# Kernel tuning notes

Hardware: AMD Instinct MI355X
Metric: run time of the kernel (lower is better)

Reference implementation:

```python
import jax, jax.numpy as jnp
import numpy as np

B, C, H, W = 8, 1, 384, 384
P, D, NH, L, E, HF = 16, 768, 12, 12, 4, 3072
Hp, Wp = H // P, W // P
N = Hp * Wp            # 576 tokens
DH = D // NH           # 64 per head
EPS = 1e-5


def setup_inputs() -> dict:
    key = jax.random.key(0)
    ks = jax.random.split(key, 10)
    g = lambda k, shp: (0.02 * jax.random.normal(k, shp, dtype=jnp.float32))
    return {
        "x": jax.random.normal(ks[0], (B, C, H, W), dtype=jnp.float32),
        "patch_w": g(ks[1], (D, C * P * P)),        # Conv2d(k=16,s=16) == unfold+matmul
        "patch_b": jnp.zeros((D,), jnp.float32),
        "pos_embed": g(ks[2], (1, N, D)),
        "ln1_g": jnp.ones((L, D), jnp.float32),
        "ln1_b": jnp.zeros((L, D), jnp.float32),
        "qkv_w": g(ks[3], (L, 3 * D, D)),           # torch MHA in_proj_weight
        "qkv_b": jnp.zeros((L, 3 * D), jnp.float32),
        "out_w": g(ks[4], (L, D, D)),
        "out_b": jnp.zeros((L, D), jnp.float32),
        "ln2_g": jnp.ones((L, D), jnp.float32),
        "ln2_b": jnp.zeros((L, D), jnp.float32),
        "gate_w": g(ks[5], (L, E, D)),
        "gate_b": jnp.zeros((L, E), jnp.float32),
        "w1": g(ks[6], (L, E, HF, D)),
        "b1": jnp.zeros((L, E, HF), jnp.float32),
        "w2": g(ks[7], (L, E, D, HF)),
        "b2": jnp.zeros((L, E, D), jnp.float32),
    }


def _ln(x, g, b):
    m = jnp.mean(x, -1, keepdims=True)
    v = jnp.var(x, -1, keepdims=True)
    return (x - m) * jax.lax.rsqrt(v + EPS) * g + b


def _layer(t, prm):
    (l1g, l1b, qw, qb, ow, ob, l2g, l2b, gw, gb, W1, B1, W2, B2) = prm
    # --- MHA (pre-LN, residual) ---
    h = _ln(t, l1g, l1b)
    qkv = h @ qw.T + qb                                   # [B,N,3D]
    q, k, v = jnp.split(qkv, 3, axis=-1)
    q = q.reshape(B, N, NH, DH).transpose(0, 2, 1, 3)     # [B,NH,N,DH]
    k = k.reshape(B, N, NH, DH).transpose(0, 2, 1, 3)
    v = v.reshape(B, N, NH, DH).transpose(0, 2, 1, 3)
    att = jax.nn.softmax(jnp.einsum('bhnd,bhmd->bhnm', q, k) / jnp.sqrt(jnp.float32(DH)), axis=-1)
    a = jnp.einsum('bhnm,bhmd->bhnd', att, v).transpose(0, 2, 1, 3).reshape(B, N, D)
    t = t + a @ ow.T + ob
    # --- MoE FFN, top_k=1: raw gate logits used as combine weights ---
    h2 = _ln(t, l2g, l2b)
    scores = h2 @ gw.T + gb                               # [B,N,E]
    idx = jnp.argmax(scores, axis=-1)                     # [B,N] chosen expert
    wgt = jnp.max(scores, axis=-1)                        # [B,N] raw logit weight
    hid = jax.nn.gelu(jnp.einsum('bnd,ehd->benh', h2, W1) + B1[None, :, None, :], approximate=False)
    y = jnp.einsum('benh,edh->bend', hid, W2) + B2[None, :, None, :]   # [B,E,N,D]
    sel = jax.nn.one_hot(idx, E, dtype=t.dtype) * wgt[..., None]       # [B,N,E]
    t = t + jnp.einsum('bend,bne->bnd', y, sel)
    return t, None


def reference(x, patch_w, patch_b, pos_embed, ln1_g, ln1_b, qkv_w, qkv_b,
              out_w, out_b, ln2_g, ln2_b, gate_w, gate_b, w1, b1, w2, b2):
    # patch embed: Conv2d(kernel=stride=P) == non-overlapping unfold + matmul
    patches = x.reshape(B, C, Hp, P, Wp, P).transpose(0, 2, 4, 1, 3, 5).reshape(B, N, C * P * P)
    tok = patches @ patch_w.T + patch_b + pos_embed
    layer = jax.checkpoint(_layer)
    tok, _ = jax.lax.scan(layer, tok,
                          (ln1_g, ln1_b, qkv_w, qkv_b, out_w, out_b,
                           ln2_g, ln2_b, gate_w, gate_b, w1, b1, w2, b2))
    # rearrange 'b (h w) c -> b c h w'
    return tok.reshape(B, Hp, Wp, D).transpose(0, 3, 1, 2)
```

## Files before the change

kernel.cpp:

```cpp
#include <hip/hip_runtime.h>
#include <cmath>

#define TOK 4608
#define DMODEL 768

typedef __attribute__((ext_vector_type(8))) _Float16 f16x8;
typedef __attribute__((ext_vector_type(4))) float f32x4;

__device__ __forceinline__ float gelu_exact(float x) {
    return 0.5f * x * (1.0f + erff(x * 0.70710678118654752440f));
}

__device__ __forceinline__ void cvt2(float x, unsigned short& h, unsigned short& m)
{
    _Float16 hf = (_Float16)x;
    float r = (x - (float)hf) * 2048.0f;
    _Float16 mf = (_Float16)r;
    h = __builtin_bit_cast(unsigned short, hf);
    m = __builtin_bit_cast(unsigned short, mf);
}

__device__ __forceinline__ void cvt2_pack8(const float4 a, const float4 b,
                                           uint4& H, uint4& M)
{
    unsigned short h[8], m[8];
    cvt2(a.x, h[0], m[0]); cvt2(a.y, h[1], m[1]);
    cvt2(a.z, h[2], m[2]); cvt2(a.w, h[3], m[3]);
    cvt2(b.x, h[4], m[4]); cvt2(b.y, h[5], m[5]);
    cvt2(b.z, h[6], m[6]); cvt2(b.w, h[7], m[7]);
    H = (uint4){ (unsigned)h[0] | ((unsigned)h[1] << 16), (unsigned)h[2] | ((unsigned)h[3] << 16),
                 (unsigned)h[4] | ((unsigned)h[5] << 16), (unsigned)h[6] | ((unsigned)h[7] << 16) };
    M = (uint4){ (unsigned)m[0] | ((unsigned)m[1] << 16), (unsigned)m[2] | ((unsigned)m[3] << 16),
                 (unsigned)m[4] | ((unsigned)m[5] << 16), (unsigned)m[6] | ((unsigned)m[7] << 16) };
}

__global__ __launch_bounds__(256)
void im2col_kernel(const float* __restrict__ x, float* __restrict__ patches)
{
    int idx = blockIdx.x*256 + threadIdx.x;
    int k = idx & 255, tokid = idx >> 8;
    int b = tokid / 576, n = tokid % 576;
    int hp = n / 24, wp = n % 24;
    patches[idx] = x[(size_t)b*147456 + (size_t)(hp*16 + (k >> 4))*384 + wp*16 + (k & 15)];
}

__global__ __launch_bounds__(256)
void ln_kernel(const float* __restrict__ in, float* __restrict__ out,
               const float* __restrict__ g, const float* __restrict__ bta)
{
    int tokid = blockIdx.x;
    const float* xr = in + (size_t)tokid*768;
    int t = threadIdx.x;
    float v0 = xr[t], v1 = xr[t+256], v2 = xr[t+512];
    float s = v0+v1+v2, q = v0*v0+v1*v1+v2*v2;
    for (int off = 32; off > 0; off >>= 1) {
        s += __shfl_down(s, off);
        q += __shfl_down(q, off);
    }
    __shared__ float ss[4], sq[4];
    int wv = t >> 6, ln = t & 63;
    if (ln == 0) { ss[wv] = s; sq[wv] = q; }
    __syncthreads();
    float ts = ss[0]+ss[1]+ss[2]+ss[3];
    float tq = sq[0]+sq[1]+sq[2]+sq[3];
    float mean = ts * (1.f/768.f);
    float var  = tq * (1.f/768.f) - mean*mean;
    float inv  = rsqrtf(var + 1e-5f);
    float* orow = out + (size_t)tokid*768;
    orow[t]     = (v0-mean)*inv*g[t]     + bta[t];
    orow[t+256] = (v1-mean)*inv*g[t+256] + bta[t+256];
    orow[t+512] = (v2-mean)*inv*g[t+512] + bta[t+512];
}

__global__ __launch_bounds__(256)
void ln2_gate_kernel(const float* __restrict__ in, float* __restrict__ out,
                     const float* __restrict__ g, const float* __restrict__ bta,
                     const float* __restrict__ gw, const float* __restrict__ gb,
                     float* __restrict__ wgt, int* __restrict__ lists,
                     int* __restrict__ counts)
{
    int tokid = blockIdx.x;
    const float* xr = in + (size_t)tokid*768;
    int t = threadIdx.x;
    float v0 = xr[t], v1 = xr[t+256], v2 = xr[t+512];
    float s = v0+v1+v2, q = v0*v0+v1*v1+v2*v2;
    for (int off = 32; off > 0; off >>= 1) {
        s += __shfl_down(s, off);
        q += __shfl_down(q, off);
    }
    __shared__ float ss[4], sq[4];
    __shared__ float red[4][4];
    int wv = t >> 6, ln = t & 63;
    if (ln == 0) { ss[wv] = s; sq[wv] = q; }
    __syncthreads();
    float ts = ss[0]+ss[1]+ss[2]+ss[3];
    float tq = sq[0]+sq[1]+sq[2]+sq[3];
    float mean = ts * (1.f/768.f);
    float var  = tq * (1.f/768.f) - mean*mean;
    float inv  = rsqrtf(var + 1e-5f);
    float y0 = (v0-mean)*inv*g[t]     + bta[t];
    float y1 = (v1-mean)*inv*g[t+256] + bta[t+256];
    float y2 = (v2-mean)*inv*g[t+512] + bta[t+512];
    float* orow = out + (size_t)tokid*768;
    orow[t] = y0; orow[t+256] = y1; orow[t+512] = y2;

    float p0, p1, p2, p3;
    p0 = fmaf(y0, gw[t], 0.f);        p0 = fmaf(y1, gw[t+256], p0);        p0 = fmaf(y2, gw[t+512], p0);
    p1 = fmaf(y0, gw[768+t], 0.f);    p1 = fmaf(y1, gw[768+t+256], p1);    p1 = fmaf(y2, gw[768+t+512], p1);
    p2 = fmaf(y0, gw[1536+t], 0.f);   p2 = fmaf(y1, gw[1536+t+256], p2);   p2 = fmaf(y2, gw[1536+t+512], p2);
    p3 = fmaf(y0, gw[2304+t], 0.f);   p3 = fmaf(y1, gw[2304+t+256], p3);   p3 = fmaf(y2, gw[2304+t+512], p3);
    for (int off = 32; off > 0; off >>= 1) {
        p0 += __shfl_down(p0, off);
        p1 += __shfl_down(p1, off);
        p2 += __shfl_down(p2, off);
        p3 += __shfl_down(p3, off);
    }
    if (ln == 0) { red[wv][0]=p0; red[wv][1]=p1; red[wv][2]=p2; red[wv][3]=p3; }
    __syncthreads();
    if (t == 0) {
        float sc[4];
        #pragma unroll
        for (int e = 0; e < 4; ++e)
            sc[e] = red[0][e]+red[1][e]+red[2][e]+red[3][e] + gb[e];
        int best = 0; float bv = sc[0];
        #pragma unroll
        for (int e = 1; e < 4; ++e) if (sc[e] > bv) { bv = sc[e]; best = e; }
        wgt[tokid] = bv;
        int pos = atomicAdd(&counts[best], 1);
        lists[best*TOK + pos] = tokid;
    }
}

template<bool SWZ>
__global__ __launch_bounds__(256, 2)
void gemm_big(const float* __restrict__ A, const float* __restrict__ Bw,
              const float* __restrict__ bias, float* __restrict__ C,
              int M, int Nout, int K, int ldA, int ldC, int mode,
              const int* __restrict__ lists, const int* __restrict__ counts,
              const float* __restrict__ wgt)
{
    int Meff = M;
    const int* gather = nullptr;
    if (counts) {
        int e = blockIdx.z;
        Meff   = counts[e];
        gather = lists + e * TOK;
        Bw    += (size_t)e * Nout * K;
        bias  += (size_t)e * Nout;
    }
    int m0, n0;
    if constexpr (SWZ) {
        int gx  = gridDim.x;
        int nwg = gx * gridDim.y;
        int bid = blockIdx.y * gx + blockIdx.x;
        bid = (bid & 7) * (nwg >> 3) + (bid >> 3);
        m0 = (bid / gx) << 7; n0 = (bid % gx) << 7;
    } else {
        m0 = blockIdx.y << 7; n0 = blockIdx.x << 7;
    }
    if (m0 >= Meff) return;

    __shared__ unsigned short Ah[128][40];
    __shared__ unsigned short Am[128][40];
    __shared__ unsigned short Bh[128][40];
    __shared__ unsigned short Bm[128][40];

    int t = threadIdx.x;
    int srow = t >> 1;
    int koff = (t & 1) << 4;

    int ar = m0 + srow;
    long agrow = -1;
    if (ar < Meff) agrow = gather ? gather[ar] : ar;
    const float* Asrc = (agrow >= 0) ? (A + (size_t)agrow*ldA + koff) : nullptr;
    const float* Bsrc = Bw + (size_t)(n0 + srow)*K + koff;

    int lane = t & 63;
    int wv   = t >> 6;
    int wm   = (wv >> 1) << 6;
    int wn   = (wv & 1) << 6;
    int r16  = lane & 15;
    int g    = lane >> 4;

    f32x4 acc1[4][4], acc2[4][4];
    #pragma unroll
    for (int i = 0; i < 4; ++i)
        #pragma unroll
        for (int j = 0; j < 4; ++j) {
            acc1[i][j] = (f32x4){0.f, 0.f, 0.f, 0.f};
            acc2[i][j] = (f32x4){0.f, 0.f, 0.f, 0.f};
        }

    float4 ra[4], rb[4];
    ra[0] = ra[1] = ra[2] = ra[3] = make_float4(0.f, 0.f, 0.f, 0.f);

    auto load_tile = [&](int k0) {
        if (Asrc) {
            ra[0] = *(const float4*)(Asrc + k0);
            ra[1] = *(const float4*)(Asrc + k0 + 4);
            ra[2] = *(const float4*)(Asrc + k0 + 8);
            ra[3] = *(const float4*)(Asrc + k0 + 12);
        }
        rb[0] = *(const float4*)(Bsrc + k0);
        rb[1] = *(const float4*)(Bsrc + k0 + 4);
        rb[2] = *(const float4*)(Bsrc + k0 + 8);
        rb[3] = *(const float4*)(Bsrc + k0 + 12);
    };

    load_tile(0);

    for (int k0 = 0; k0 < K; k0 += 32) {
        __syncthreads();
        {
            uint4 H, M_;
            cvt2_pack8(ra[0], ra[1], H, M_);
            *(uint4*)&Ah[srow][koff]   = H;
            *(uint4*)&Am[srow][koff]   = M_;
            cvt2_pack8(ra[2], ra[3], H, M_);
            *(uint4*)&Ah[srow][koff+8] = H;
            *(uint4*)&Am[srow][koff+8] = M_;
            cvt2_pack8(rb[0], rb[1], H, M_);
            *(uint4*)&Bh[srow][koff]   = H;
            *(uint4*)&Bm[srow][koff]   = M_;
            cvt2_pack8(rb[2], rb[3], H, M_);
            *(uint4*)&Bh[srow][koff+8] = H;
            *(uint4*)&Bm[srow][koff+8] = M_;
        }
        __syncthreads();
        if (k0 + 32 < K) load_tile(k0 + 32);

        f16x8 fah[4], fam[4];
        #pragma unroll
        for (int i = 0; i < 4; ++i) {
            int ml = wm + i*16 + r16;
            fah[i] = *(const f16x8*)&Ah[ml][g*8];
            fam[i] = *(const f16x8*)&Am[ml][g*8];
        }
        #pragma unroll
        for (int j = 0; j < 4; ++j) {
            int nl = wn + j*16 + r16;
            f16x8 fbh = *(const f16x8*)&Bh[nl][g*8];
            f16x8 fbm = *(const f16x8*)&Bm[nl][g*8];
            #pragma unroll
            for (int i = 0; i < 4; ++i) {
                acc1[i][j] = __builtin_amdgcn_mfma_f32_16x16x32_f16(fah[i], fbh, acc1[i][j], 0, 0, 0);
                acc2[i][j] = __builtin_amdgcn_mfma_f32_16x16x32_f16(fah[i], fbm, acc2[i][j], 0, 0, 0);
                acc2[i][j] = __builtin_amdgcn_mfma_f32_16x16x32_f16(fam[i], fbh, acc2[i][j], 0, 0, 0);
            }
        }
    }

    const float MS = 1.0f / 2048.0f;
    float biasv[4];
    #pragma unroll
    for (int j = 0; j < 4; ++j) biasv[j] = bias[n0 + wn + j*16 + r16];

    #pragma unroll
    for (int i = 0; i < 4; ++i) {
        int mb = m0 + wm + i*16 + (g << 2);
        #pragma unroll
        for (int r = 0; r < 4; ++r) {
            int m = mb + r;
            if (m >= Meff) continue;
            int row = gather ? gather[m] : m;
            size_t rowoff = (size_t)row*ldC + n0 + wn + r16;
            float w = (mode == 3) ? wgt[row] : 0.f;
            #pragma unroll
            for (int j = 0; j < 4; ++j) {
                float val = acc1[i][j][r] + acc2[i][j][r] * MS + biasv[j];
                size_t off = rowoff + j*16;
                if      (mode == 0) C[off] = val;
                else if (mode == 1) C[off] += val;
                else if (mode == 2) C[off] = gelu_exact(val);
                else if (mode == 3) C[off] += w * val;
                else C[off] = val + wgt[(size_t)(row % 576)*768 + n0 + wn + j*16 + r16];
            }
        }
    }
}

template<bool SWZ>
__global__ __launch_bounds__(256, 2)
void gemm_small(const float* __restrict__ A, const float* __restrict__ Bw,
                const float* __restrict__ bias, float* __restrict__ C,
                int M, int Nout, int K, int ldA, int ldC, int mode,
                const int* __restrict__ lists, const int* __restrict__ counts,
                const float* __restrict__ wgt)
{
    int Meff = M;
    const int* gather = nullptr;
    if (counts) {
        int e = blockIdx.z;
        Meff   = counts[e];
        gather = lists + e * TOK;
        Bw    += (size_t)e * Nout * K;
        bias  += (size_t)e * Nout;
    }
    int m0, n0;
    if constexpr (SWZ) {
        int gx  = gridDim.x;
        int nwg = gx * gridDim.y;
        int bid = blockIdx.y * gx + blockIdx.x;
        bid = (bid & 7) * (nwg >> 3) + (bid >> 3);
        m0 = (bid / gx) << 6; n0 = (bid % gx) << 6;
    } else {
        m0 = blockIdx.y << 6; n0 = blockIdx.x << 6;
    }
    if (m0 >= Meff) return;

    __shared__ unsigned short Ah[64][72];
    __shared__ unsigned short Am[64][72];
    __shared__ unsigned short Bh[64][72];
    __shared__ unsigned short Bm[64][72];

    int t = threadIdx.x;
    int srow  = t >> 1;
    int khalf = (t & 1) << 5;
    bool isA = srow < 64;
    int row  = isA ? srow : (srow - 64);

    const float* src = nullptr;
    if (isA) {
        int ar = m0 + row;
        if (ar < Meff) {
            long agrow = gather ? gather[ar] : ar;
            src = A + (size_t)agrow*ldA + khalf;
        }
    } else {
        src = Bw + (size_t)(n0 + row)*K + khalf;
    }

    int lane = t & 63;
    int wv   = t >> 6;
    int wm   = (wv >> 1) << 5;
    int wn   = (wv & 1) << 5;
    int r16  = lane & 15;
    int g    = lane >> 4;

    f32x4 acc1[2][2], acc2[2][2];
    #pragma unroll
    for (int i = 0; i < 2; ++i)
        #pragma unroll
        for (int j = 0; j < 2; ++j) {
            acc1[i][j] = (f32x4){0.f, 0.f, 0.f, 0.f};
            acc2[i][j] = (f32x4){0.f, 0.f, 0.f, 0.f};
        }

    float4 rr[8];
    #pragma unroll
    for (int i = 0; i < 8; ++i) rr[i] = make_float4(0.f, 0.f, 0.f, 0.f);

    auto load_tile = [&](int k0) {
        if (src) {
            #pragma unroll
            for (int i = 0; i < 8; ++i) rr[i] = *(const float4*)(src + k0 + 4*i);
        }
    };

    load_tile(0);

    for (int k0 = 0; k0 < K; k0 += 64) {
        __syncthreads();
        {
            unsigned short (*Xh)[72] = isA ? Ah : Bh;
            unsigned short (*Xm)[72] = isA ? Am : Bm;
            #pragma unroll
            for (int i = 0; i < 8; i += 2) {
                uint4 H, M_;
                cvt2_pack8(rr[i], rr[i+1], H, M_);
                *(uint4*)&Xh[row][khalf + 4*i] = H;
                *(uint4*)&Xm[row][khalf + 4*i] = M_;
            }
        }
        __syncthreads();
        if (k0 + 64 < K) load_tile(k0 + 64);

        #pragma unroll
        for (int ks = 0; ks < 2; ++ks) {
            f16x8 fah[2], fam[2];
            #pragma unroll
            for (int i = 0; i < 2; ++i) {
                int ml = wm + i*16 + r16;
                fah[i] = *(const f16x8*)&Ah[ml][ks*32 + g*8];
                fam[i] = *(const f16x8*)&Am[ml][ks*32 + g*8];
            }
            #pragma unroll
            for (int j = 0; j < 2; ++j) {
                int nl = wn + j*16 + r16;
                f16x8 fbh = *(const f16x8*)&Bh[nl][ks*32 + g*8];
                f16x8 fbm = *(const f16x8*)&Bm[nl][ks*32 + g*8];
                #pragma unroll
                for (int i = 0; i < 2; ++i) {
                    acc1[i][j] = __builtin_amdgcn_mfma_f32_16x16x32_f16(fah[i], fbh, acc1[i][j], 0, 0, 0);
                    acc2[i][j] = __builtin_amdgcn_mfma_f32_16x16x32_f16(fah[i], fbm, acc2[i][j], 0, 0, 0);
                    acc2[i][j] = __builtin_amdgcn_mfma_f32_16x16x32_f16(fam[i], fbh, acc2[i][j], 0, 0, 0);
                }
            }
        }
    }

    const float MS = 1.0f / 2048.0f;
    float biasv[2];
    #pragma unroll
    for (int j = 0; j < 2; ++j) biasv[j] = bias[n0 + wn + j*16 + r16];

    #pragma unroll
    for (int i = 0; i < 2; ++i) {
        int mb = m0 + wm + i*16 + (g << 2);
        #pragma unroll
        for (int r = 0; r < 4; ++r) {
            int m = mb + r;
            if (m >= Meff) continue;
            int rowc = gather ? gather[m] : m;
            size_t rowoff = (size_t)rowc*ldC + n0 + wn + r16;
            float w = (mode == 3) ? wgt[rowc] : 0.f;
            #pragma unroll
            for (int j = 0; j < 2; ++j) {
                float val = acc1[i][j][r] + acc2[i][j][r] * MS + biasv[j];
                size_t off = rowoff + j*16;
                if      (mode == 0) C[off] = val;
                else if (mode == 1) C[off] += val;
                else if (mode == 2) C[off] = gelu_exact(val);
                else if (mode == 3) C[off] += w * val;
                else C[off] = val + wgt[(size_t)(rowc % 576)*768 + n0 + wn + j*16 + r16];
            }
        }
    }
}

__global__ __launch_bounds__(256)
void attn_kernel(const float* __restrict__ qkv, float* __restrict__ attn)
{
    int q0 = blockIdx.x << 6;
    int h  = blockIdx.y;
    int b  = blockIdx.z;
    const float* base = qkv + (size_t)b * 576 * 2304;
    int qoff = h << 6, koff = 768 + (h << 6), voff = 1536 + (h << 6);

    __shared__ unsigned short Qh[64][72], Qm[64][72];
    __shared__ unsigned short Kh[64][72], Km[64][72];
    __shared__ unsigned short Vth[64][72], Vtm[64][72];
    __shared__ unsigned short Ph[64][72], Pm[64][72];

    int t    = threadIdx.x;
    int lane = t & 63;
    int wq   = t >> 6;
    int l15  = lane & 15;
    int g    = lane >> 4;

    int srow = t >> 2;
    int sq   = t & 3;

    {
        const float* src = &base[(size_t)(q0 + srow)*2304 + qoff + (sq << 4)];
        #pragma unroll
        for (int k = 0; k < 16; k += 4) {
            float4 v = *(const float4*)(src + k);
            ushort4 hh, mm;
            cvt2(v.x, hh.x, mm.x); cvt2(v.y, hh.y, mm.y);
            cvt2(v.z, hh.z, mm.z); cvt2(v.w, hh.w, mm.w);
            *(ushort4*)&Qh[srow][(sq << 4) + k] = hh;
            *(ushort4*)&Qm[srow][(sq << 4) + k] = mm;
        }
    }
    __syncthreads();

    f16x8 fqh[2], fqm[2];
    #pragma unroll
    for (int ks = 0; ks < 2; ++ks) {
        fqh[ks] = *(const f16x8*)&Qh[wq*16 + l15][ks*32 + g*8];
        fqm[ks] = *(const f16x8*)&Qm[wq*16 + l15][ks*32 + g*8];
    }

    float4 rk[4], rv[4];
    {
        const float* ks_ = &base[(size_t)srow*2304 + koff + (sq << 4)];
        const float* vs_ = &base[(size_t)srow*2304 + voff + (sq << 2)];
        #pragma unroll
        for (int k = 0; k < 4; ++k) rk[k] = *(const float4*)(ks_ + 4*k);
        #pragma unroll
        for (int k = 0; k < 4; ++k) rv[k] = *(const float4*)(vs_ + 16*k);
    }

    f32x4 o1[4], o2[4];
    #pragma unroll
    for (int df = 0; df < 4; ++df) {
        o1[df] = (f32x4){0.f,0.f,0.f,0.f};
        o2[df] = (f32x4){0.f,0.f,0.f,0.f};
    }
    float m_[4] = {-3.4e38f,-3.4e38f,-3.4e38f,-3.4e38f};
    float l_[4] = {0.f,0.f,0.f,0.f};
    const float MS = 1.0f / 2048.0f;

    for (int j0 = 0; j0 < 576; j0 += 64) {
        __syncthreads();
        #pragma unroll
        for (int k = 0; k < 4; ++k) {
            ushort4 hh, mm;
            cvt2(rk[k].x, hh.x, mm.x); cvt2(rk[k].y, hh.y, mm.y);
            cvt2(rk[k].z, hh.z, mm.z); cvt2(rk[k].w, hh.w, mm.w);
            *(ushort4*)&Kh[srow][(sq << 4) + 4*k] = hh;
            *(ushort4*)&Km[srow][(sq << 4) + 4*k] = mm;
        }
        #pragma unroll
        for (int k = 0; k < 4; ++k) {
            ushort4 hh, mm;
            cvt2(rv[k].x, hh.x, mm.x); cvt2(rv[k].y, hh.y, mm.y);
            cvt2(rv[k].z, hh.z, mm.z); cvt2(rv[k].w, hh.w, mm.w);
            int dbase = (sq << 2) + (k << 4);
            Vth[dbase+0][srow] = hh.x; Vtm[dbase+0][srow] = mm.x;
            Vth[dbase+1][srow] = hh.y; Vtm[dbase+1][srow] = mm.y;
            Vth[dbase+2][srow] = hh.z; Vtm[dbase+2][srow] = mm.z;
            Vth[dbase+3][srow] = hh.w; Vtm[dbase+3][srow] = mm.w;
        }
        __syncthreads();
        int jn = j0 + 64;
        if (jn < 576) {
            const float* ks_ = &base[(size_t)(jn + srow)*2304 + koff + (sq << 4)];
            const float* vs_ = &base[(size_t)(jn + srow)*2304 + voff + (sq << 2)];
            #pragma unroll
            for (int k = 0; k < 4; ++k) rk[k] = *(const float4*)(ks_ + 4*k);
            #pragma unroll
            for (int k = 0; k < 4; ++k) rv[k] = *(const float4*)(vs_ + 16*k);
        }

        f32x4 s1[4], s2[4];
        #pragma unroll
        for (int jf = 0; jf < 4; ++jf) {
            s1[jf] = (f32x4){0.f,0.f,0.f,0.f};
            s2[jf] = (f32x4){0.f,0.f,0.f,0.f};
        }
        #pragma unroll
        for (int jf = 0; jf < 4; ++jf) {
            #pragma unroll
            for (int ks = 0; ks < 2; ++ks) {
                f16x8 fkh = *(const f16x8*)&Kh[jf*16 + l15][ks*32 + g*8];
                f16x8 fkm = *(const f16x8*)&Km[jf*16 + l15][ks*32 + g*8];
                s1[jf] = __builtin_amdgcn_mfma_f32_16x16x32_f16(fqh[ks], fkh, s1[jf], 0, 0, 0);
                s2[jf] = __builtin_amdgcn_mfma_f32_16x16x32_f16(fqh[ks], fkm, s2[jf], 0, 0, 0);
                s2[jf] = __builtin_amdgcn_mfma_f32_16x16x32_f16(fqm[ks], fkh, s2[jf], 0, 0, 0);
            }
        }
        float p[4][4];
        #pragma unroll
        for (int jf = 0; jf < 4; ++jf)
            #pragma unroll
            for (int r = 0; r < 4; ++r)
                p[jf][r] = (s1[jf][r] + s2[jf][r]*MS) * 0.125f;

        #pragma unroll
        for (int r = 0; r < 4; ++r) {
            float tm = fmaxf(fmaxf(p[0][r], p[1][r]), fmaxf(p[2][r], p[3][r]));
            #pragma unroll
            for (int off = 8; off > 0; off >>= 1) tm = fmaxf(tm, __shfl_xor(tm, off, 16));
            float mn = fmaxf(m_[r], tm);
            float f  = expf(m_[r] - mn);
            m_[r] = mn;
            l_[r] *= f;
            #pragma unroll
            for (int df = 0; df < 4; ++df) { o1[df][r] *= f; o2[df][r] *= f; }
            float ps = 0.f;
            #pragma unroll
            for (int jf = 0; jf < 4; ++jf) {
                p[jf][r] = expf(p[jf][r] - mn);
                ps += p[jf][r];
            }
            #pragma unroll
            for (int off = 8; off > 0; off >>= 1) ps += __shfl_xor(ps, off, 16);
            l_[r] += ps;
        }
        #pragma unroll
        for (int jf = 0; jf < 4; ++jf)
            #pragma unroll
            for (int r = 0; r < 4; ++r) {
                unsigned short ph, pm;
                cvt2(p[jf][r], ph, pm);
                Ph[wq*16 + g*4 + r][jf*16 + l15] = ph;
                Pm[wq*16 + g*4 + r][jf*16 + l15] = pm;
            }

        #pragma unroll
        for (int ks = 0; ks < 2; ++ks) {
            f16x8 fph = *(const f16x8*)&Ph[wq*16 + l15][ks*32 + g*8];
            f16x8 fpm = *(const f16x8*)&Pm[wq*16 + l15][ks*32 + g*8];
            #pragma unroll
            for (int df = 0; df < 4; ++df) {
                f16x8 fvh = *(const f16x8*)&Vth[df*16 + l15][ks*32 + g*8];
                f16x8 fvm = *(const f16x8*)&Vtm[df*16 + l15][ks*32 + g*8];
                o1[df] = __builtin_amdgcn_mfma_f32_16x16x32_f16(fph, fvh, o1[df], 0, 0, 0);
                o2[df] = __builtin_amdgcn_mfma_f32_16x16x32_f16(fph, fvm, o2[df], 0, 0, 0);
                o2[df] = __builtin_amdgcn_mfma_f32_16x16x32_f16(fpm, fvh, o2[df], 0, 0, 0);
            }
        }
    }

    #pragma unroll
    for (int r = 0; r < 4; ++r) {
        float inv = 1.f / l_[r];
        size_t row = (size_t)(b*576 + q0 + wq*16 + g*4 + r)*768 + qoff + l15;
        #pragma unroll
        for (int df = 0; df < 4; ++df)
            attn[row + df*16] = (o1[df][r] + o2[df][r]*MS) * inv;
    }
}

__global__ void zero_counts48(int* counts) { if (threadIdx.x < 48) counts[threadIdx.x] = 0; }

__global__ __launch_bounds__(256)
void out_transpose(const float* __restrict__ tok, float* __restrict__ out)
{
    int idx = blockIdx.x*256 + threadIdx.x;
    int wp = idx % 24;
    int hp = (idx / 24) % 24;
    int d  = (idx / 576) % 768;
    int b  = idx / (576*768);
    out[idx] = tok[(size_t)(b*576 + hp*24 + wp)*768 + d];
}

extern "C" void kernel_launch(void* const* d_in, const int* in_sizes, int n_in,
                              void* d_out, int out_size, void* d_ws, size_t ws_size,
                              hipStream_t stream)
{
    const float* x       = (const float*)d_in[0];
    const float* patch_w = (const float*)d_in[1];
    const float* patch_b = (const float*)d_in[2];
    const float* pos     = (const float*)d_in[3];
    const float* ln1_g   = (const float*)d_in[4];
    const float* ln1_b   = (const float*)d_in[5];
    const float* qkv_w   = (const float*)d_in[6];
    const float* qkv_b   = (const float*)d_in[7];
    const float* out_w   = (const float*)d_in[8];
    const float* out_b   = (const float*)d_in[9];
    const float* ln2_g   = (const float*)d_in[10];
    const float* ln2_b   = (const float*)d_in[11];
    const float* gate_w  = (const float*)d_in[12];
    const float* gate_b  = (const float*)d_in[13];
    const float* w1      = (const float*)d_in[14];
    const float* b1      = (const float*)d_in[15];
    const float* w2      = (const float*)d_in[16];
    const float* b2      = (const float*)d_in[17];
    float* out = (float*)d_out;

    float* ws    = (float*)d_ws;
    float* tok   = ws;
    float* h     = ws + 3538944;
    float* scr   = ws + 7077888;
    float* qkv   = scr;
    float* attn  = scr + 10616832;
    float* hid   = scr;
    float* patches = scr;
    float* wgt   = ws + 21233664;
    int*   lists = (int*)(ws + 21238272);
    int*   counts= (int*)(ws + 21256704);

    zero_counts48<<<1, 64, 0, stream>>>(counts);

    im2col_kernel<<<4608, 256, 0, stream>>>(x, patches);
    gemm_small<true><<<dim3(12,72,1), 256, 0, stream>>>(patches, patch_w, patch_b, tok,
                                                        4608, 768, 256, 256, 768, 4,
                                                        nullptr, nullptr, pos);

    for (int l = 0; l < 12; ++l) {
        int* counts_l = counts + l*4;
        ln_kernel<<<4608, 256, 0, stream>>>(tok, h, ln1_g + l*768, ln1_b + l*768);
        gemm_big<true><<<dim3(18,36,1), 256, 0, stream>>>(h, qkv_w + (size_t)l*1769472,
                                                          qkv_b + l*2304, qkv,
                                                          4608, 2304, 768, 768, 2304, 0,
                                                          nullptr, nullptr, nullptr);
        attn_kernel<<<dim3(9,12,8), 256, 0, stream>>>(qkv, attn);
        gemm_small<true><<<dim3(12,72,1), 256, 0, stream>>>(attn, out_w + (size_t)l*589824,
                                                            out_b + l*768, tok,
                                                            4608, 768, 768, 768, 768, 1,
                                                            nullptr, nullptr, nullptr);
        ln2_gate_kernel<<<4608, 256, 0, stream>>>(tok, h, ln2_g + l*768, ln2_b + l*768,
                                                  gate_w + l*3072, gate_b + l*4,
                                                  wgt, lists, counts_l);
        gemm_big<false><<<dim3(24,36,4), 256, 0, stream>>>(h, w1 + (size_t)l*9437184,
                                                           b1 + (size_t)l*4*3072, hid,
                                                           4608, 3072, 768, 768, 3072, 2,
                                                           lists, counts_l, nullptr);
        gemm_small<false><<<dim3(12,72,4), 256, 0, stream>>>(hid, w2 + (size_t)l*9437184,
                                                             b2 + (size_t)l*4*768, tok,
                                                             4608, 768, 3072, 3072, 768, 3,
                                                             lists, counts_l, wgt);
    }
    out_transpose<<<13824, 256, 0, stream>>>(tok, out);
}
```

Measured before the change: 8.169 ms.

## Replace GEMM kernels with 256x128-tile 512-thread wide GEMM for all layer matmuls

Replaces the 128x128-tile, 256-thread GEMM with a 256x128-tile, 512-thread variant (8 waves) that reuses each B tile across twice as many rows. It is used for the QKV, out-projection and both MoE expert GEMMs, replacing gemm_small for the N=768 cases. The XCD swizzle is generalised to grids whose block count is not a multiple of 8. The intent is fewer B reloads and less per-block overhead, at the cost of more LDS per block, fewer blocks for the N=768 GEMMs, and more wasted rows on partially filled expert tiles.

```diff
diff --git a/kernel.cpp b/kernel.cpp
--- a/kernel.cpp
+++ b/kernel.cpp
@@ -132,12 +132,12 @@
 }
 
 template<bool SWZ>
-__global__ __launch_bounds__(256, 2)
-void gemm_big(const float* __restrict__ A, const float* __restrict__ Bw,
-              const float* __restrict__ bias, float* __restrict__ C,
-              int M, int Nout, int K, int ldA, int ldC, int mode,
-              const int* __restrict__ lists, const int* __restrict__ counts,
-              const float* __restrict__ wgt)
+__global__ __launch_bounds__(512, 2)
+void gemm_wide(const float* __restrict__ A, const float* __restrict__ Bw,
+               const float* __restrict__ bias, float* __restrict__ C,
+               int M, int Nout, int K, int ldA, int ldC, int mode,
+               const int* __restrict__ lists, const int* __restrict__ counts,
+               const float* __restrict__ wgt)
 {
     int Meff = M;
     const int* gather = nullptr;
@@ -148,32 +148,34 @@
         Bw    += (size_t)e * Nout * K;
         bias  += (size_t)e * Nout;
     }
-    int m0, n0;
+    int gx  = gridDim.x;
+    int bid = blockIdx.y * gx + blockIdx.x;
     if constexpr (SWZ) {
-        int gx  = gridDim.x;
         int nwg = gx * gridDim.y;
-        int bid = blockIdx.y * gx + blockIdx.x;
-        bid = (bid & 7) * (nwg >> 3) + (bid >> 3);
-        m0 = (bid / gx) << 7; n0 = (bid % gx) << 7;
-    } else {
-        m0 = blockIdx.y << 7; n0 = blockIdx.x << 7;
-    }
+        int qq = nwg >> 3, rr8 = nwg & 7;
+        int xcd = bid & 7, idx = bid >> 3;
+        bid = (xcd < rr8 ? xcd*(qq+1) : rr8*(qq+1) + (xcd-rr8)*qq) + idx;
+    }
+    int m0 = (bid / gx) << 8;
+    int n0 = (bid % gx) << 7;
     if (m0 >= Meff) return;
 
-    __shared__ unsigned short Ah[128][40];
-    __shared__ unsigned short Am[128][40];
+    __shared__ unsigned short Ah[256][40];
+    __shared__ unsigned short Am[256][40];
     __shared__ unsigned short Bh[128][40];
     __shared__ unsigned short Bm[128][40];
 
     int t = threadIdx.x;
-    int srow = t >> 1;
-    int koff = (t & 1) << 4;
+    int srow  = t >> 1;
+    int koff  = (t & 1) << 4;
+    int brow  = t >> 2;
+    int bkoff = (t & 3) << 3;
 
     int ar = m0 + srow;
     long agrow = -1;
     if (ar < Meff) agrow = gather ? gather[ar] : ar;
     const float* Asrc = (agrow >= 0) ? (A + (size_t)agrow*ldA + koff) : nullptr;
-    const float* Bsrc = Bw + (size_t)(n0 + srow)*K + koff;
+    const float* Bsrc = Bw + (size_t)(n0 + brow)*K + bkoff;
 
     int lane = t & 63;
     int wv   = t >> 6;
@@ -191,7 +193,7 @@
             acc2[i][j] = (f32x4){0.f, 0.f, 0.f, 0.f};
         }
 
-    float4 ra[4], rb[4];
+    float4 ra[4], rb0, rb1;
     ra[0] = ra[1] = ra[2] = ra[3] = make_float4(0.f, 0.f, 0.f, 0.f);
 
     auto load_tile = [&](int k0) {
@@ -201,10 +203,8 @@
             ra[2] = *(const float4*)(Asrc + k0 + 8);
             ra[3] = *(const float4*)(Asrc + k0 + 12);
         }
-        rb[0] = *(const float4*)(Bsrc + k0);
-        rb[1] = *(const float4*)(Bsrc + k0 + 4);
-        rb[2] = *(const float4*)(Bsrc + k0 + 8);
-        rb[3] = *(const float4*)(Bsrc + k0 + 12);
+        rb0 = *(const float4*)(Bsrc + k0);
+        rb1 = *(const float4*)(Bsrc + k0 + 4);
     };
 
     load_tile(0);
@@ -219,12 +219,9 @@
             cvt2_pack8(ra[2], ra[3], H, M_);
             *(uint4*)&Ah[srow][koff+8] = H;
             *(uint4*)&Am[srow][koff+8] = M_;
-            cvt2_pack8(rb[0], rb[1], H, M_);
-            *(uint4*)&Bh[srow][koff]   = H;
-            *(uint4*)&Bm[srow][koff]   = M_;
-            cvt2_pack8(rb[2], rb[3], H, M_);
-            *(uint4*)&Bh[srow][koff+8] = H;
-            *(uint4*)&Bm[srow][koff+8] = M_;
+            cvt2_pack8(rb0, rb1, H, M_);
+            *(uint4*)&Bh[brow][bkoff]  = H;
+            *(uint4*)&Bm[brow][bkoff]  = M_;
         }
         __syncthreads();
         if (k0 + 32 < K) load_tile(k0 + 32);
@@ -272,8 +269,7 @@
                 if      (mode == 0) C[off] = val;
                 else if (mode == 1) C[off] += val;
                 else if (mode == 2) C[off] = gelu_exact(val);
-                else if (mode == 3) C[off] += w * val;
-                else C[off] = val + wgt[(size_t)(row % 576)*768 + n0 + wn + j*16 + r16];
+                else                C[off] += w * val;
             }
         }
     }
@@ -663,26 +659,26 @@
     for (int l = 0; l < 12; ++l) {
         int* counts_l = counts + l*4;
         ln_kernel<<<4608, 256, 0, stream>>>(tok, h, ln1_g + l*768, ln1_b + l*768);
-        gemm_big<true><<<dim3(18,36,1), 256, 0, stream>>>(h, qkv_w + (size_t)l*1769472,
-                                                          qkv_b + l*2304, qkv,
-                                                          4608, 2304, 768, 768, 2304, 0,
+        gemm_wide<true><<<dim3(18,18,1), 512, 0, stream>>>(h, qkv_w + (size_t)l*1769472,
+                                                           qkv_b + l*2304, qkv,
+                                                           4608, 2304, 768, 768, 2304, 0,
+                                                           nullptr, nullptr, nullptr);
+        attn_kernel<<<dim3(9,12,8), 256, 0, stream>>>(qkv, attn);
+        gemm_wide<true><<<dim3(6,18,1), 512, 0, stream>>>(attn, out_w + (size_t)l*589824,
+                                                          out_b + l*768, tok,
+                                                          4608, 768, 768, 768, 768, 1,
                                                           nullptr, nullptr, nullptr);
-        attn_kernel<<<dim3(9,12,8), 256, 0, stream>>>(qkv, attn);
-        gemm_small<true><<<dim3(12,72,1), 256, 0, stream>>>(attn, out_w + (size_t)l*589824,
-                                                            out_b + l*768, tok,
-                                                            4608, 768, 768, 768, 768, 1,
-                                                            nullptr, nullptr, nullptr);
         ln2_gate_kernel<<<4608, 256, 0, stream>>>(tok, h, ln2_g + l*768, ln2_b + l*768,
                                                   gate_w + l*3072, gate_b + l*4,
                                                   wgt, lists, counts_l);
-        gemm_big<false><<<dim3(24,36,4), 256, 0, stream>>>(h, w1 + (size_t)l*9437184,
-                                                           b1 + (size_t)l*4*3072, hid,
-                                                           4608, 3072, 768, 768, 3072, 2,
-                                                           lists, counts_l, nullptr);
-        gemm_small<false><<<dim3(12,72,4), 256, 0, stream>>>(hid, w2 + (size_t)l*9437184,
-                                                             b2 + (size_t)l*4*768, tok,
-                                                             4608, 768, 3072, 3072, 768, 3,
-                                                             lists, counts_l, wgt);
+        gemm_wide<false><<<dim3(24,18,4), 512, 0, stream>>>(h, w1 + (size_t)l*9437184,
+                                                            b1 + (size_t)l*4*3072, hid,
+                                                            4608, 3072, 768, 768, 3072, 2,
+                                                            lists, counts_l, nullptr);
+        gemm_wide<false><<<dim3(6,18,4), 512, 0, stream>>>(hid, w2 + (size_t)l*9437184,
+                                                           b2 + (size_t)l*4*768, tok,
+                                                           4608, 768, 3072, 3072, 768, 3,
+                                                           lists, counts_l, wgt);
     }
     out_transpose<<<13824, 256, 0, stream>>>(tok, out);
 }
```

Measured after the change: 8.319 ms. About the same (+1.8%).
